# Kernel tuning notes

Measured on AMD Instinct MI355X. Metric: run time of the kernel, lower is better.

The kernel has to match this reference:

```python
import jax, jax.numpy as jnp
import numpy as np

N_NODES = 100000
D_IN = 128
D_OUT = 128
N_REL = 4
N_EDGES = 500000


def setup_inputs() -> dict:
    key = jax.random.key(0)
    k_x, k_e, k_w, k_b, k_ws, k_bs = jax.random.split(key, 6)
    x = jax.random.normal(k_x, (N_NODES, D_IN), dtype=jnp.float32)
    # edge_indices[r] = [2, E]: row 0 = source node ids, row 1 = target node ids
    edge_indices = jax.random.randint(k_e, (N_REL, 2, N_EDGES), 0, N_NODES, dtype=jnp.int32)
    scale = 1.0 / np.sqrt(D_IN)
    # per-relation Linear weights (out, in) and biases, like nn.Linear
    W = jax.random.uniform(k_w, (N_REL, D_OUT, D_IN), dtype=jnp.float32, minval=-scale, maxval=scale)
    b = jax.random.uniform(k_b, (N_REL, D_OUT), dtype=jnp.float32, minval=-scale, maxval=scale)
    W_sl = jax.random.uniform(k_ws, (D_OUT, D_IN), dtype=jnp.float32, minval=-scale, maxval=scale)
    b_sl = jax.random.uniform(k_bs, (D_OUT,), dtype=jnp.float32, minval=-scale, maxval=scale)
    return {"x": x, "edge_indices": edge_indices, "W": W, "b": b, "W_sl": W_sl, "b_sl": b_sl}


def reference(x, edge_indices, W, b, W_sl, b_sl):
    # gather source features per relation: [R, E, D_IN]
    src = edge_indices[:, 0]  # [R, E]
    tgt = edge_indices[:, 1]  # [R, E]
    xs = x[src]  # [R, E, D_IN]
    # per-relation linear (nn.Linear: x @ W.T + b): [R, E, D_OUT]
    msgs = jnp.einsum('red,rfd->ref', xs, W) + b[:, None, :]
    # scatter-add into per-relation node accumulators, then sum over relations
    agg = jax.vmap(lambda m, t: jax.ops.segment_sum(m, t, num_segments=N_NODES))(msgs, tgt)
    agg = agg.sum(axis=0)  # [N, D_OUT]
    # self loop
    agg = agg + x @ W_sl.T + b_sl
    return agg
```

## Files before the change

### kernel.cpp

```cpp
#include <hip/hip_runtime.h>
#include <hip/hip_bf16.h>

#define N_NODES 100000
#define D 128
#define N_REL 4
#define N_EDGES 500000
#define N_CNT (N_REL * N_NODES)
#define SCAN_CHUNK 1024
#define N_SCAN_BLK ((N_CNT + SCAN_CHUNK - 1) / SCAN_CHUNK)

typedef __attribute__((ext_vector_type(8))) short bf16x8;
typedef __attribute__((ext_vector_type(4))) float f32x4;

__device__ __forceinline__ unsigned short f2bf(float f) {
    unsigned int u = __float_as_uint(f);
    u += 0x7fffu + ((u >> 16) & 1u);
    return (unsigned short)(u >> 16);
}

#define CVT_BLOCKS 6250
#define WB_BLOCKS 320
#define HIST_BLOCKS 7813
__global__ __launch_bounds__(256) void prep_kernel(const float* __restrict__ x,
                                                   const int* __restrict__ ei,
                                                   const float* __restrict__ W,
                                                   const float* __restrict__ W_sl,
                                                   ushort* __restrict__ xbf,
                                                   ushort* __restrict__ WbT,
                                                   int* __restrict__ cnt) {
    const int b = blockIdx.x, tid = threadIdx.x;
    if (b < CVT_BLOCKS) {
        size_t t = (size_t)b * 256 + tid;
        float4 v0 = ((const float4*)x)[t * 2];
        float4 v1 = ((const float4*)x)[t * 2 + 1];
        int4 o;
        o.x = ((int)f2bf(v0.y) << 16) | f2bf(v0.x);
        o.y = ((int)f2bf(v0.w) << 16) | f2bf(v0.z);
        o.z = ((int)f2bf(v1.y) << 16) | f2bf(v1.x);
        o.w = ((int)f2bf(v1.w) << 16) | f2bf(v1.z);
        ((int4*)xbf)[t] = o;
    } else if (b < CVT_BLOCKS + WB_BLOCKS) {
        int t = (b - CVT_BLOCKS) * 256 + tid;
        int f = t / 640;
        int k = t - f * 640;
        float v;
        if (k < 512) {
            int r = k >> 7, d = k & 127;
            v = W[((size_t)r * 128 + f) * 128 + d];
        } else {
            v = W_sl[(size_t)f * 128 + (k - 512)];
        }
        WbT[t] = f2bf(v);
    } else {
        int t = (b - CVT_BLOCKS - WB_BLOCKS) * 256 + tid;
        if (t >= N_REL * N_EDGES) return;
        int r = t / N_EDGES;
        int e = t - r * N_EDGES;
        int tgt = ei[(size_t)r * 2 * N_EDGES + N_EDGES + e];
        atomicAdd(&cnt[r * N_NODES + tgt], 1);
    }
}

__global__ __launch_bounds__(256) void scanA(const int* __restrict__ cnt,
                                             int* __restrict__ off,
                                             int* __restrict__ partials) {
    __shared__ int ps[256];
    int b = blockIdx.x, t = threadIdx.x;
    int i0 = b * SCAN_CHUNK + t * 4;
    int v[4];
#pragma unroll
    for (int q = 0; q < 4; ++q) v[q] = (i0 + q < N_CNT) ? cnt[i0 + q] : 0;
    int s = v[0] + v[1] + v[2] + v[3];
    ps[t] = s;
    __syncthreads();
    for (int d = 1; d < 256; d <<= 1) {
        int u = (t >= d) ? ps[t - d] : 0;
        __syncthreads();
        ps[t] += u;
        __syncthreads();
    }
    if (t == 255) partials[b] = ps[255];
    int run = (t == 0) ? 0 : ps[t - 1];
#pragma unroll
    for (int q = 0; q < 4; ++q) {
        if (i0 + q < N_CNT) off[i0 + q] = run;
        run += v[q];
    }
}
__global__ __launch_bounds__(512) void scanB(int* __restrict__ partials) {
    __shared__ int ps[512];
    int t = threadIdx.x;
    ps[t] = (t < N_SCAN_BLK) ? partials[t] : 0;
    __syncthreads();
    for (int d = 1; d < 512; d <<= 1) {
        int u = (t >= d) ? ps[t - d] : 0;
        __syncthreads();
        ps[t] += u;
        __syncthreads();
    }
    if (t < N_SCAN_BLK) partials[t] = (t == 0) ? 0 : ps[t - 1];
}

__global__ __launch_bounds__(256) void bucket_kernel(const int* __restrict__ ei,
                                                     const int* __restrict__ off,
                                                     const int* __restrict__ partials,
                                                     int* __restrict__ cur0,
                                                     int* __restrict__ sorted) {
    int t = blockIdx.x * 256 + threadIdx.x;
    if (t >= N_REL * N_EDGES) return;
    int r = t / N_EDGES;
    int e = t - r * N_EDGES;
    int src = ei[(size_t)r * 2 * N_EDGES + e];
    int tgt = ei[(size_t)r * 2 * N_EDGES + N_EDGES + e];
    int i = r * N_NODES + tgt;
    int pos = off[i] + partials[i >> 10] + atomicAdd(&cur0[i], 1);
    sorted[pos] = src;
}

__global__ __launch_bounds__(512) void gather_kernel(const ushort* __restrict__ xbf,
                                                     const int* __restrict__ sorted,
                                                     const int* __restrict__ off,
                                                     const int* __restrict__ partials,
                                                     const int* __restrict__ cnt,
                                                     unsigned int* __restrict__ buf) {
    const int p = blockIdx.x * 8 + (threadIdx.x >> 6);
    const int lane = threadIdx.x & 63;
    int base = __builtin_amdgcn_readfirstlane(off[p] + partials[p >> 10]);
    int c = __builtin_amdgcn_readfirstlane(cnt[p]);
    float ax = 0.f, ay = 0.f;
    int j = 0;
    for (; j + 4 <= c; j += 4) {
        int s0 = sorted[base + j + 0];
        int s1 = sorted[base + j + 1];
        int s2 = sorted[base + j + 2];
        int s3 = sorted[base + j + 3];
        unsigned int u0 = ((const unsigned int*)(xbf + ((size_t)s0 << 7)))[lane];
        unsigned int u1 = ((const unsigned int*)(xbf + ((size_t)s1 << 7)))[lane];
        unsigned int u2 = ((const unsigned int*)(xbf + ((size_t)s2 << 7)))[lane];
        unsigned int u3 = ((const unsigned int*)(xbf + ((size_t)s3 << 7)))[lane];
        ax += __uint_as_float(u0 << 16) + __uint_as_float(u1 << 16)
            + __uint_as_float(u2 << 16) + __uint_as_float(u3 << 16);
        ay += __uint_as_float(u0 & 0xffff0000u) + __uint_as_float(u1 & 0xffff0000u)
            + __uint_as_float(u2 & 0xffff0000u) + __uint_as_float(u3 & 0xffff0000u);
    }
    for (; j < c; ++j) {
        int s0 = sorted[base + j];
        unsigned int u0 = ((const unsigned int*)(xbf + ((size_t)s0 << 7)))[lane];
        ax += __uint_as_float(u0 << 16);
        ay += __uint_as_float(u0 & 0xffff0000u);
    }
    buf[(size_t)p * 64 + lane] = ((unsigned int)f2bf(ay) << 16) | f2bf(ax);
}

__global__ __launch_bounds__(256) void gemm_kernel(const ushort* __restrict__ buf,
                                                   const ushort* __restrict__ xbf,
                                                   const ushort* __restrict__ WbT,
                                                   const int* __restrict__ cnt,
                                                   const float* __restrict__ bias,
                                                   const float* __restrict__ b_sl,
                                                   float* __restrict__ out) {
    __shared__ __align__(16) ushort As[128 * 72];
    __shared__ __align__(16) ushort Bs[128 * 72];
    __shared__ float degS[4 * 128];
    __shared__ float biasS[4 * 128];
    __shared__ float bslS[128];

    const int tid = threadIdx.x;
    const int l = tid & 63, w = tid >> 6;
    const int wr = w >> 1, wc = w & 1;
    const int lr = l & 15, lq = l >> 4;
    const int n0 = blockIdx.x * 128;

#pragma unroll
    for (int it = 0; it < 2; ++it) {
        int idx = it * 256 + tid;
        int r = idx >> 7, row = idx & 127;
        int n = n0 + row;
        degS[idx] = (n < N_NODES) ? (float)cnt[r * N_NODES + n] : 0.f;
        biasS[idx] = bias[idx];
    }
    if (tid < 128) bslS[tid] = b_sl[tid];

    f32x4 acc[4][4];
#pragma unroll
    for (int mi = 0; mi < 4; ++mi)
#pragma unroll
        for (int ni = 0; ni < 4; ++ni) acc[mi][ni] = (f32x4){0.f, 0.f, 0.f, 0.f};

    for (int kt = 0; kt < 10; ++kt) {
        __syncthreads();
        const int region = kt >> 1;
        const int d0 = (kt & 1) * 64;
#pragma unroll
        for (int it = 0; it < 4; ++it) {
            int id = it * 256 + tid;
            int r_ = id >> 3, c16 = id & 7;
            int n = n0 + r_;
            if (n > N_NODES - 1) n = N_NODES - 1;
            const ushort* sp = (region < 4)
                ? ((const ushort*)buf + (((size_t)region * N_NODES + n) << 7) + d0)
                : (xbf + ((size_t)n << 7) + d0);
            int4 v = *(const int4*)(sp + c16 * 8);
            *(int4*)(As + r_ * 72 + c16 * 8) = v;
        }
#pragma unroll
        for (int it = 0; it < 4; ++it) {
            int id = it * 256 + tid;
            int f_ = id >> 3, c16 = id & 7;
            int4 v = *(const int4*)(WbT + (size_t)f_ * 640 + kt * 64 + c16 * 8);
            *(int4*)(Bs + f_ * 72 + c16 * 8) = v;
        }
        __syncthreads();
#pragma unroll
        for (int ks = 0; ks < 2; ++ks) {
            bf16x8 a[4], bb[4];
#pragma unroll
            for (int mi = 0; mi < 4; ++mi)
                a[mi] = *(const bf16x8*)(As + (wr * 64 + mi * 16 + lr) * 72 + ks * 32 + lq * 8);
#pragma unroll
            for (int ni = 0; ni < 4; ++ni)
                bb[ni] = *(const bf16x8*)(Bs + (wc * 64 + ni * 16 + lr) * 72 + ks * 32 + lq * 8);
#pragma unroll
            for (int mi = 0; mi < 4; ++mi)
#pragma unroll
                for (int ni = 0; ni < 4; ++ni)
                    acc[mi][ni] = __builtin_amdgcn_mfma_f32_16x16x32_bf16(a[mi], bb[ni], acc[mi][ni], 0, 0, 0);
        }
    }

    float bw[4][4], bsl_[4];
#pragma unroll
    for (int ni = 0; ni < 4; ++ni) {
        int f = wc * 64 + ni * 16 + lr;
        bsl_[ni] = bslS[f];
#pragma unroll
        for (int r = 0; r < 4; ++r) bw[ni][r] = biasS[r * 128 + f];
    }
#pragma unroll
    for (int mi = 0; mi < 4; ++mi) {
#pragma unroll
        for (int q = 0; q < 4; ++q) {
            int row = wr * 64 + mi * 16 + lq * 4 + q;
            int n = n0 + row;
            if (n >= N_NODES) continue;
            float d0_ = degS[row], d1_ = degS[128 + row], d2_ = degS[256 + row], d3_ = degS[384 + row];
#pragma unroll
            for (int ni = 0; ni < 4; ++ni) {
                int f = wc * 64 + ni * 16 + lr;
                float v = acc[mi][ni][q] + d0_ * bw[ni][0] + d1_ * bw[ni][1]
                        + d2_ * bw[ni][2] + d3_ * bw[ni][3] + bsl_[ni];
                out[(size_t)n * 128 + f] = v;
            }
        }
    }
}

extern "C" void kernel_launch(void* const* d_in, const int* in_sizes, int n_in,
                              void* d_out, int out_size, void* d_ws, size_t ws_size,
                              hipStream_t stream) {
    const float* x    = (const float*)d_in[0];
    const int*   ei   = (const int*)d_in[1];
    const float* W    = (const float*)d_in[2];
    const float* b    = (const float*)d_in[3];
    const float* W_sl = (const float*)d_in[4];
    const float* b_sl = (const float*)d_in[5];
    float* out = (float*)d_out;

    int*          cnt      = (int*)d_ws;
    int*          cur0     = cnt + N_CNT;
    int*          off      = cur0 + N_CNT;
    int*          partials = off + N_CNT;
    ushort*       WbT      = (ushort*)(partials + 512);
    ushort*       xbf      = WbT + 128 * 640;
    int*          sorted   = (int*)(xbf + (size_t)N_NODES * D);
    unsigned int* buf      = (unsigned int*)(sorted + N_REL * N_EDGES);

    hipMemsetAsync(cnt, 0, 2 * N_CNT * sizeof(int), stream);

    prep_kernel<<<CVT_BLOCKS + WB_BLOCKS + HIST_BLOCKS, 256, 0, stream>>>(x, ei, W, W_sl, xbf, WbT, cnt);
    scanA<<<N_SCAN_BLK, 256, 0, stream>>>(cnt, off, partials);
    scanB<<<1, 512, 0, stream>>>(partials);
    bucket_kernel<<<(N_REL * N_EDGES + 255) / 256, 256, 0, stream>>>(ei, off, partials, cur0, sorted);
    gather_kernel<<<N_CNT / 8, 512, 0, stream>>>(xbf, sorted, off, partials, cnt, buf);
    gemm_kernel<<<(N_NODES + 127) / 128, 256, 0, stream>>>((const ushort*)buf, xbf, WbT, cnt, b, b_sl, out);
}
```

Measured before the change: 439.7 us.

## Pad CSR buckets to multiples of four and prefetch GEMM tiles in registers

The per-(relation, node) edge buckets are now padded to multiples of four. Padding slots point at a new all-zero sentinel row of the bf16 feature table, and the partial-sum fold moves into a new scanC kernel that also resets the cursors. Each gather wave handles four bucket rows using int4 index loads with no tail loop, and no longer reads cnt or partials. The GEMM now loads the next K tile into registers while MFMAs run on the current tile. The goal is lower per-bucket overhead and hidden global load latency, at the cost of an extra kernel launch and many wasted sentinel loads, since average bucket sizes are small.

```diff
diff --git a/kernel.cpp b/kernel.cpp
--- a/kernel.cpp
+++ b/kernel.cpp
@@ -8,6 +8,7 @@
 #define N_CNT (N_REL * N_NODES)
 #define SCAN_CHUNK 1024
 #define N_SCAN_BLK ((N_CNT + SCAN_CHUNK - 1) / SCAN_CHUNK)
+#define SORT_MAX (N_REL * N_EDGES + 3 * N_CNT)
 
 typedef __attribute__((ext_vector_type(8))) short bf16x8;
 typedef __attribute__((ext_vector_type(4))) float f32x4;
@@ -20,6 +21,7 @@
 
 #define CVT_BLOCKS 6250
 #define WB_BLOCKS 320
+#define ZR_BLOCKS 1
 #define HIST_BLOCKS 7813
 __global__ __launch_bounds__(256) void prep_kernel(const float* __restrict__ x,
                                                    const int* __restrict__ ei,
@@ -51,8 +53,10 @@
             v = W_sl[(size_t)f * 128 + (k - 512)];
         }
         WbT[t] = f2bf(v);
+    } else if (b < CVT_BLOCKS + WB_BLOCKS + ZR_BLOCKS) {
+        if (tid < 16) ((uint4*)(xbf + (size_t)N_NODES * D))[tid] = make_uint4(0, 0, 0, 0);
     } else {
-        int t = (b - CVT_BLOCKS - WB_BLOCKS) * 256 + tid;
+        int t = (b - CVT_BLOCKS - WB_BLOCKS - ZR_BLOCKS) * 256 + tid;
         if (t >= N_REL * N_EDGES) return;
         int r = t / N_EDGES;
         int e = t - r * N_EDGES;
@@ -62,14 +66,14 @@
 }
 
 __global__ __launch_bounds__(256) void scanA(const int* __restrict__ cnt,
-                                             int* __restrict__ off,
+                                             int* __restrict__ foff,
                                              int* __restrict__ partials) {
     __shared__ int ps[256];
     int b = blockIdx.x, t = threadIdx.x;
     int i0 = b * SCAN_CHUNK + t * 4;
     int v[4];
 #pragma unroll
-    for (int q = 0; q < 4; ++q) v[q] = (i0 + q < N_CNT) ? cnt[i0 + q] : 0;
+    for (int q = 0; q < 4; ++q) v[q] = (i0 + q < N_CNT) ? ((cnt[i0 + q] + 3) & ~3) : 0;
     int s = v[0] + v[1] + v[2] + v[3];
     ps[t] = s;
     __syncthreads();
@@ -83,11 +87,12 @@
     int run = (t == 0) ? 0 : ps[t - 1];
 #pragma unroll
     for (int q = 0; q < 4; ++q) {
-        if (i0 + q < N_CNT) off[i0 + q] = run;
+        if (i0 + q < N_CNT) foff[i0 + q] = run;
         run += v[q];
     }
 }
-__global__ __launch_bounds__(512) void scanB(int* __restrict__ partials) {
+__global__ __launch_bounds__(512) void scanB(int* __restrict__ partials,
+                                             int* __restrict__ foff) {
     __shared__ int ps[512];
     int t = threadIdx.x;
     ps[t] = (t < N_SCAN_BLK) ? partials[t] : 0;
@@ -99,11 +104,25 @@
         __syncthreads();
     }
     if (t < N_SCAN_BLK) partials[t] = (t == 0) ? 0 : ps[t - 1];
+    if (t == N_SCAN_BLK - 1) foff[N_CNT] = ps[t];
+}
+__global__ __launch_bounds__(256) void scanC(int* __restrict__ foff,
+                                             const int* __restrict__ partials,
+                                             const int* __restrict__ cnt,
+                                             int* __restrict__ cur0,
+                                             int* __restrict__ sorted) {
+    int i = blockIdx.x * 256 + threadIdx.x;
+    if (i >= N_CNT) return;
+    int base = foff[i] + partials[i >> 10];
+    foff[i] = base;
+    cur0[i] = 0;
+    int c = cnt[i];
+    int cp = (c + 3) & ~3;
+    for (int j = c; j < cp; ++j) sorted[base + j] = N_NODES;
 }
 
 __global__ __launch_bounds__(256) void bucket_kernel(const int* __restrict__ ei,
-                                                     const int* __restrict__ off,
-                                                     const int* __restrict__ partials,
+                                                     const int* __restrict__ foff,
                                                      int* __restrict__ cur0,
                                                      int* __restrict__ sorted) {
     int t = blockIdx.x * 256 + threadIdx.x;
@@ -113,43 +132,37 @@
     int src = ei[(size_t)r * 2 * N_EDGES + e];
     int tgt = ei[(size_t)r * 2 * N_EDGES + N_EDGES + e];
     int i = r * N_NODES + tgt;
-    int pos = off[i] + partials[i >> 10] + atomicAdd(&cur0[i], 1);
+    int pos = foff[i] + atomicAdd(&cur0[i], 1);
     sorted[pos] = src;
 }
 
-__global__ __launch_bounds__(512) void gather_kernel(const ushort* __restrict__ xbf,
+__global__ __launch_bounds__(256) void gather_kernel(const ushort* __restrict__ xbf,
                                                      const int* __restrict__ sorted,
-                                                     const int* __restrict__ off,
-                                                     const int* __restrict__ partials,
-                                                     const int* __restrict__ cnt,
+                                                     const int* __restrict__ foff,
                                                      unsigned int* __restrict__ buf) {
-    const int p = blockIdx.x * 8 + (threadIdx.x >> 6);
+    int wid = (blockIdx.x * 256 + threadIdx.x) >> 6;
+    wid = __builtin_amdgcn_readfirstlane(wid);
     const int lane = threadIdx.x & 63;
-    int base = __builtin_amdgcn_readfirstlane(off[p] + partials[p >> 10]);
-    int c = __builtin_amdgcn_readfirstlane(cnt[p]);
-    float ax = 0.f, ay = 0.f;
-    int j = 0;
-    for (; j + 4 <= c; j += 4) {
-        int s0 = sorted[base + j + 0];
-        int s1 = sorted[base + j + 1];
-        int s2 = sorted[base + j + 2];
-        int s3 = sorted[base + j + 3];
-        unsigned int u0 = ((const unsigned int*)(xbf + ((size_t)s0 << 7)))[lane];
-        unsigned int u1 = ((const unsigned int*)(xbf + ((size_t)s1 << 7)))[lane];
-        unsigned int u2 = ((const unsigned int*)(xbf + ((size_t)s2 << 7)))[lane];
-        unsigned int u3 = ((const unsigned int*)(xbf + ((size_t)s3 << 7)))[lane];
-        ax += __uint_as_float(u0 << 16) + __uint_as_float(u1 << 16)
-            + __uint_as_float(u2 << 16) + __uint_as_float(u3 << 16);
-        ay += __uint_as_float(u0 & 0xffff0000u) + __uint_as_float(u1 & 0xffff0000u)
-            + __uint_as_float(u2 & 0xffff0000u) + __uint_as_float(u3 & 0xffff0000u);
-    }
-    for (; j < c; ++j) {
-        int s0 = sorted[base + j];
-        unsigned int u0 = ((const unsigned int*)(xbf + ((size_t)s0 << 7)))[lane];
-        ax += __uint_as_float(u0 << 16);
-        ay += __uint_as_float(u0 & 0xffff0000u);
-    }
-    buf[(size_t)p * 64 + lane] = ((unsigned int)f2bf(ay) << 16) | f2bf(ax);
+    const int p0 = wid * 4;
+    int f0 = foff[p0], f1 = foff[p0 + 1], f2 = foff[p0 + 2], f3 = foff[p0 + 3], f4 = foff[p0 + 4];
+#pragma unroll
+    for (int pi = 0; pi < 4; ++pi) {
+        int gb = (pi == 0) ? f0 : (pi == 1) ? f1 : (pi == 2) ? f2 : f3;
+        int ge = (pi == 0) ? f1 : (pi == 1) ? f2 : (pi == 2) ? f3 : f4;
+        float ax = 0.f, ay = 0.f;
+        for (int g = gb; g < ge; g += 4) {
+            int4 s = *(const int4*)(sorted + g);
+            unsigned int u0 = ((const unsigned int*)(xbf + ((size_t)s.x << 7)))[lane];
+            unsigned int u1 = ((const unsigned int*)(xbf + ((size_t)s.y << 7)))[lane];
+            unsigned int u2 = ((const unsigned int*)(xbf + ((size_t)s.z << 7)))[lane];
+            unsigned int u3 = ((const unsigned int*)(xbf + ((size_t)s.w << 7)))[lane];
+            ax += __uint_as_float(u0 << 16) + __uint_as_float(u1 << 16)
+                + __uint_as_float(u2 << 16) + __uint_as_float(u3 << 16);
+            ay += __uint_as_float(u0 & 0xffff0000u) + __uint_as_float(u1 & 0xffff0000u)
+                + __uint_as_float(u2 & 0xffff0000u) + __uint_as_float(u3 & 0xffff0000u);
+        }
+        buf[(size_t)(p0 + pi) * 64 + lane] = ((unsigned int)f2bf(ay) << 16) | f2bf(ax);
+    }
 }
 
 __global__ __launch_bounds__(256) void gemm_kernel(const ushort* __restrict__ buf,
@@ -187,8 +200,10 @@
 #pragma unroll
         for (int ni = 0; ni < 4; ++ni) acc[mi][ni] = (f32x4){0.f, 0.f, 0.f, 0.f};
 
-    for (int kt = 0; kt < 10; ++kt) {
-        __syncthreads();
+    const int ar_ = (tid * 4) >> 3 >> 0;
+    int4 aReg[4], bReg[4];
+
+    auto LOAD = [&](int kt) {
         const int region = kt >> 1;
         const int d0 = (kt & 1) * 64;
 #pragma unroll
@@ -200,17 +215,28 @@
             const ushort* sp = (region < 4)
                 ? ((const ushort*)buf + (((size_t)region * N_NODES + n) << 7) + d0)
                 : (xbf + ((size_t)n << 7) + d0);
-            int4 v = *(const int4*)(sp + c16 * 8);
-            *(int4*)(As + r_ * 72 + c16 * 8) = v;
+            aReg[it] = *(const int4*)(sp + c16 * 8);
         }
 #pragma unroll
         for (int it = 0; it < 4; ++it) {
             int id = it * 256 + tid;
             int f_ = id >> 3, c16 = id & 7;
-            int4 v = *(const int4*)(WbT + (size_t)f_ * 640 + kt * 64 + c16 * 8);
-            *(int4*)(Bs + f_ * 72 + c16 * 8) = v;
-        }
-        __syncthreads();
+            bReg[it] = *(const int4*)(WbT + (size_t)f_ * 640 + kt * 64 + c16 * 8);
+        }
+    };
+
+    LOAD(0);
+    for (int kt = 0; kt < 10; ++kt) {
+        __syncthreads();
+#pragma unroll
+        for (int it = 0; it < 4; ++it) {
+            int id = it * 256 + tid;
+            int r_ = id >> 3, c16 = id & 7;
+            *(int4*)(As + r_ * 72 + c16 * 8) = aReg[it];
+            *(int4*)(Bs + r_ * 72 + c16 * 8) = bReg[it];
+        }
+        __syncthreads();
+        if (kt < 9) LOAD(kt + 1);
 #pragma unroll
         for (int ks = 0; ks < 2; ++ks) {
             bf16x8 a[4], bb[4];
@@ -268,19 +294,21 @@
 
     int*          cnt      = (int*)d_ws;
     int*          cur0     = cnt + N_CNT;
-    int*          off      = cur0 + N_CNT;
-    int*          partials = off + N_CNT;
+    int*          foff     = cur0 + N_CNT;
+    int*          partials = foff + N_CNT + 64;
     ushort*       WbT      = (ushort*)(partials + 512);
     ushort*       xbf      = WbT + 128 * 640;
-    int*          sorted   = (int*)(xbf + (size_t)N_NODES * D);
-    unsigned int* buf      = (unsigned int*)(sorted + N_REL * N_EDGES);
-
-    hipMemsetAsync(cnt, 0, 2 * N_CNT * sizeof(int), stream);
-
-    prep_kernel<<<CVT_BLOCKS + WB_BLOCKS + HIST_BLOCKS, 256, 0, stream>>>(x, ei, W, W_sl, xbf, WbT, cnt);
-    scanA<<<N_SCAN_BLK, 256, 0, stream>>>(cnt, off, partials);
-    scanB<<<1, 512, 0, stream>>>(partials);
-    bucket_kernel<<<(N_REL * N_EDGES + 255) / 256, 256, 0, stream>>>(ei, off, partials, cur0, sorted);
-    gather_kernel<<<N_CNT / 8, 512, 0, stream>>>(xbf, sorted, off, partials, cnt, buf);
+    int*          sorted   = (int*)(xbf + (size_t)(N_NODES + 1) * D + 64);
+    unsigned int* buf      = (unsigned int*)(sorted + SORT_MAX);
+
+    hipMemsetAsync(cnt, 0, N_CNT * sizeof(int), stream);
+
+    prep_kernel<<<CVT_BLOCKS + WB_BLOCKS + ZR_BLOCKS + HIST_BLOCKS, 256, 0, stream>>>(
+        x, ei, W, W_sl, xbf, WbT, cnt);
+    scanA<<<N_SCAN_BLK, 256, 0, stream>>>(cnt, foff, partials);
+    scanB<<<1, 512, 0, stream>>>(partials, foff);
+    scanC<<<(N_CNT + 255) / 256, 256, 0, stream>>>(foff, partials, cnt, cur0, sorted);
+    bucket_kernel<<<(N_REL * N_EDGES + 255) / 256, 256, 0, stream>>>(ei, foff, cur0, sorted);
+    gather_kernel<<<N_CNT / 16, 256, 0, stream>>>(xbf, sorted, foff, buf);
     gemm_kernel<<<(N_NODES + 127) / 128, 256, 0, stream>>>((const ushort*)buf, xbf, WbT, cnt, b, b_sl, out);
 }
```

Measured after the change: 483.3 us. 9.9% more time.
